# Performance work log

Hardware: AMD Instinct MI355X
Metric: run time of the kernel (lower is better)

## Reference

```python
import jax, jax.numpy as jnp
import numpy as np

FILTERS = 512
DQK = FILTERS // 8  # 64


def setup_inputs() -> dict:
    key = jax.random.key(0)
    ks = jax.random.split(key, 7)
    B, H, W, C = 32, 32, 32, FILTERS
    x = jax.random.normal(ks[0], (B, H, W, C), dtype=jnp.float32)
    # 1x1 convs == per-pixel dense layers: weight [Cin, Cout], bias [Cout]
    def glorot(k, cin, cout):
        lim = np.sqrt(6.0 / (cin + cout)).astype(np.float32)
        return jax.random.uniform(k, (cin, cout), jnp.float32, -lim, lim)
    return {
        "x": x,
        "wq": glorot(ks[1], C, DQK), "bq": jnp.zeros((DQK,), jnp.float32),
        "wk": glorot(ks[2], C, DQK), "bk": jnp.zeros((DQK,), jnp.float32),
        "wv": glorot(ks[3], C, C),   "bv": jnp.zeros((C,), jnp.float32),
    }


def reference(x, wq, bq, wk, bk, wv, bv):
    B, H, W, C = x.shape
    N = H * W
    xf = x.reshape(B, N, C)                       # flatten spatial -> tokens
    q = xf @ wq + bq                              # [B, N, C//8]
    k = xf @ wk + bk                              # [B, N, C//8]
    v = xf @ wv + bv                              # [B, N, C]
    scale = 1.0 / jnp.sqrt(jnp.float32(C // 8))
    scores = jnp.einsum('bnd,bmd->bnm', q, k) * scale  # [B, N, N]
    probs = jax.nn.softmax(scores, axis=-1)
    attended = jnp.einsum('bnm,bmc->bnc', probs, v)    # [B, N, C]
    return attended.reshape(B, H, W, C) + x
```

## Files before the change

### kernel.cpp

```cpp
#include <hip/hip_runtime.h>
#include <stdint.h>

#define B_ 32
#define N_ 1024
#define C_ 512
#define D_ 64

typedef __attribute__((ext_vector_type(8))) __bf16 bf8;
typedef __attribute__((ext_vector_type(4))) float f32x4;

typedef const __attribute__((address_space(1))) void* gp_t;
typedef __attribute__((address_space(3))) void* lp_t;

__device__ inline void g2l16(const void* g, void* l) {
    __builtin_amdgcn_global_load_lds((gp_t)g, (lp_t)l, 16, 0, 0);
}

__device__ inline float b2f(unsigned short u) {
    return __uint_as_float(((unsigned)u) << 16);
}
__device__ inline unsigned short f2b(float f) {
    unsigned u = __float_as_uint(f);
    u += 0x7FFF + ((u >> 16) & 1);
    return (unsigned short)(u >> 16);
}

#define MFMA16(a, b, c) __builtin_amdgcn_mfma_f32_16x16x32_bf16((a), (b), (c), 0, 0, 0)

__global__ __launch_bounds__(256) void xcvt(const float* __restrict__ x,
                                            unsigned short* __restrict__ xb) {
    int i = blockIdx.x * 256 + threadIdx.x;
    float4 f = ((const float4*)x)[i];
    ushort4 o;
    o.x = f2b(f.x); o.y = f2b(f.y); o.z = f2b(f.z); o.w = f2b(f.w);
    ((ushort4*)xb)[i] = o;
}

__global__ __launch_bounds__(256) void wtrans(const float* __restrict__ w,
                                              unsigned short* __restrict__ wt,
                                              int cout) {
    int t = blockIdx.x * 256 + threadIdx.x;
    int co = t >> 9;
    int ci = t & 511;
    wt[t] = f2b(w[(size_t)ci * cout + co]);
}

__global__ __launch_bounds__(256) void qkv(
    const unsigned short* __restrict__ xb,
    const unsigned short* __restrict__ WT,
    const float* __restrict__ bq, const float* __restrict__ bk,
    const float* __restrict__ bv,
    unsigned short* __restrict__ q, unsigned short* __restrict__ k,
    unsigned short* __restrict__ vT)
{
    const int rb = blockIdx.x;
    const int cb = blockIdx.y;
    const int tid = threadIdx.x;
    const int lane = tid & 63;
    const int wave = tid >> 6;
    const int wm = wave >> 1, wn = wave & 1;
    const int lr = lane & 15;
    const int lk = lane >> 4;

    __shared__ unsigned short SM[16896];
    unsigned short* As = SM;
    unsigned short* Bs = SM + 8192;
    unsigned short* TB = SM;

    const int row0 = rb * 128;
    const int col0 = cb * 128;

    f32x4 zero4 = {0.f, 0.f, 0.f, 0.f};
    f32x4 acc[4][4];
    #pragma unroll
    for (int i = 0; i < 4; ++i)
        #pragma unroll
        for (int j = 0; j < 4; ++j) acc[i][j] = zero4;

    for (int kk = 0; kk < C_; kk += 64) {
        __syncthreads();
        #pragma unroll
        for (int i = 0; i < 4; ++i) {
            int f = wave * 4 + i;
            int t = f >> 1, kq = f & 1;
            g2l16(xb + (size_t)(row0 + t * 16 + lr) * C_ + kk + kq * 32 + lk * 8,
                  &As[f * 512]);
            g2l16(WT + (size_t)(col0 + t * 16 + lr) * C_ + kk + kq * 32 + lk * 8,
                  &Bs[f * 512]);
        }
        __syncthreads();
        #pragma unroll
        for (int kq = 0; kq < 2; ++kq) {
            bf8 a[4], bb[4];
            #pragma unroll
            for (int ti = 0; ti < 4; ++ti)
                a[ti] = *(const bf8*)&As[((wm * 4 + ti) * 2 + kq) * 512 + lane * 8];
            #pragma unroll
            for (int tj = 0; tj < 4; ++tj)
                bb[tj] = *(const bf8*)&Bs[((wn * 4 + tj) * 2 + kq) * 512 + lane * 8];
            #pragma unroll
            for (int ti = 0; ti < 4; ++ti)
                #pragma unroll
                for (int tj = 0; tj < 4; ++tj)
                    acc[ti][tj] = MFMA16(a[ti], bb[tj], acc[ti][tj]);
        }
    }

    if (cb == 0) {
        unsigned short* outp = (wn == 0) ? q : k;
        const float* bias = (wn == 0) ? bq : bk;
        #pragma unroll
        for (int ti = 0; ti < 4; ++ti)
            #pragma unroll
            for (int tj = 0; tj < 4; ++tj) {
                int col = tj * 16 + lr;
                float bi = bias[col];
                #pragma unroll
                for (int r = 0; r < 4; ++r) {
                    int row = row0 + wm * 64 + ti * 16 + lk * 4 + r;
                    outp[(size_t)row * D_ + col] = f2b(acc[ti][tj][r] + bi);
                }
            }
    } else {
        const int colv = (cb - 1) * 128;
        __syncthreads();
        #pragma unroll
        for (int ti = 0; ti < 4; ++ti)
            #pragma unroll
            for (int tj = 0; tj < 4; ++tj) {
                int c = wn * 64 + tj * 16 + lr;
                float bi = bv[colv + c];
                int tok = wm * 64 + ti * 16 + lk * 4;
                ushort4 o;
                o.x = f2b(acc[ti][tj][0] + bi);
                o.y = f2b(acc[ti][tj][1] + bi);
                o.z = f2b(acc[ti][tj][2] + bi);
                o.w = f2b(acc[ti][tj][3] + bi);
                *(ushort4*)&TB[c * 132 + tok] = o;
            }
        __syncthreads();
        const int b  = row0 >> 10;
        const int n0 = row0 & 1023;
        #pragma unroll
        for (int i = 0; i < 16; ++i) {
            int idx = tid + 256 * i;
            int c = idx >> 5, ch = idx & 31;
            ushort4 t4 = *(const ushort4*)&TB[c * 132 + ch * 4];
            *(ushort4*)&vT[((size_t)(b * C_ + colv + c)) * N_ + n0 + ch * 4] = t4;
        }
    }
}

#define SLD 1032
__global__ __launch_bounds__(256) void scores(
    const unsigned short* __restrict__ q,
    const unsigned short* __restrict__ k,
    unsigned short* __restrict__ P)
{
    const int qt = blockIdx.x, b = blockIdx.y;
    const int tid = threadIdx.x, lane = tid & 63, wave = tid >> 6;
    const int lr = lane & 15, lk = lane >> 4;
    __shared__ unsigned short S[16 * SLD];

    const int n0 = qt * 16;
    const unsigned short* qrow = q + (size_t)(b * N_ + n0 + lr) * D_ + lk * 8;
    bf8 qa0 = *(const bf8*)(qrow);
    bf8 qa1 = *(const bf8*)(qrow + 32);

    const int m0w = wave * 256;
    #pragma unroll 4
    for (int mt = 0; mt < 16; ++mt) {
        int m = m0w + mt * 16;
        const unsigned short* krow = k + (size_t)(b * N_ + m + lr) * D_ + lk * 8;
        bf8 kb0 = *(const bf8*)(krow);
        bf8 kb1 = *(const bf8*)(krow + 32);
        f32x4 s = {0.f, 0.f, 0.f, 0.f};
        s = MFMA16(qa0, kb0, s);
        s = MFMA16(qa1, kb1, s);
        #pragma unroll
        for (int r = 0; r < 4; ++r)
            S[(lk * 4 + r) * SLD + m + lr] = f2b(s[r] * 0.125f);
    }
    __syncthreads();

    #pragma unroll
    for (int rr4 = 0; rr4 < 4; ++rr4) {
        int rr = wave * 4 + rr4;
        float vals[16];
        float mx = -1e30f;
        #pragma unroll
        for (int j = 0; j < 16; ++j) {
            vals[j] = b2f(S[rr * SLD + j * 64 + lane]);
            mx = fmaxf(mx, vals[j]);
        }
        #pragma unroll
        for (int off = 32; off; off >>= 1) mx = fmaxf(mx, __shfl_xor(mx, off));
        float sum = 0.f;
        #pragma unroll
        for (int j = 0; j < 16; ++j) { vals[j] = __expf(vals[j] - mx); sum += vals[j]; }
        #pragma unroll
        for (int off = 32; off; off >>= 1) sum += __shfl_xor(sum, off);
        float inv = 1.f / sum;
        unsigned short* pp = P + (size_t)(b * N_ + n0 + rr) * N_;
        #pragma unroll
        for (int j = 0; j < 16; ++j) pp[j * 64 + lane] = f2b(vals[j] * inv);
    }
}

__global__ __launch_bounds__(256) void pv(
    const unsigned short* __restrict__ P,
    const unsigned short* __restrict__ vT,
    const float* __restrict__ x,
    float* __restrict__ out)
{
    const int m0 = blockIdx.x * 128, c0 = blockIdx.y * 128, b = blockIdx.z;
    const int tid = threadIdx.x, lane = tid & 63, wave = tid >> 6;
    const int wm = wave >> 1, wn = wave & 1;
    const int lr = lane & 15, lk = lane >> 4;

    __shared__ unsigned short As[128 * 64];
    __shared__ unsigned short Bs[128 * 64];

    f32x4 zero4 = {0.f, 0.f, 0.f, 0.f};
    f32x4 acc[4][4];
    #pragma unroll
    for (int i = 0; i < 4; ++i)
        #pragma unroll
        for (int j = 0; j < 4; ++j) acc[i][j] = zero4;

    const unsigned short* Pb = P  + (size_t)b * N_ * N_;
    const unsigned short* Vb = vT + (size_t)b * C_ * N_;

    for (int kk = 0; kk < N_; kk += 64) {
        __syncthreads();
        #pragma unroll
        for (int i = 0; i < 4; ++i) {
            int f = wave * 4 + i;
            int t = f >> 1, kq = f & 1;
            g2l16(Pb + (size_t)(m0 + t * 16 + lr) * N_ + kk + kq * 32 + lk * 8,
                  &As[f * 512]);
            g2l16(Vb + (size_t)(c0 + t * 16 + lr) * N_ + kk + kq * 32 + lk * 8,
                  &Bs[f * 512]);
        }
        __syncthreads();
        #pragma unroll
        for (int kq = 0; kq < 2; ++kq) {
            bf8 a[4], bb[4];
            #pragma unroll
            for (int ti = 0; ti < 4; ++ti)
                a[ti] = *(const bf8*)&As[((wm * 4 + ti) * 2 + kq) * 512 + lane * 8];
            #pragma unroll
            for (int tj = 0; tj < 4; ++tj)
                bb[tj] = *(const bf8*)&Bs[((wn * 4 + tj) * 2 + kq) * 512 + lane * 8];
            #pragma unroll
            for (int ti = 0; ti < 4; ++ti)
                #pragma unroll
                for (int tj = 0; tj < 4; ++tj)
                    acc[ti][tj] = MFMA16(a[ti], bb[tj], acc[ti][tj]);
        }
    }

    #pragma unroll
    for (int ti = 0; ti < 4; ++ti)
        #pragma unroll
        for (int tj = 0; tj < 4; ++tj) {
            int col = c0 + wn * 64 + tj * 16 + lr;
            #pragma unroll
            for (int r = 0; r < 4; ++r) {
                int row = m0 + wm * 64 + ti * 16 + lk * 4 + r;
                size_t idx = (size_t)(b * N_ + row) * C_ + col;
                out[idx] = acc[ti][tj][r] + x[idx];
            }
        }
}

extern "C" void kernel_launch(void* const* d_in, const int* in_sizes, int n_in,
                              void* d_out, int out_size, void* d_ws, size_t ws_size,
                              hipStream_t stream) {
    (void)in_sizes; (void)n_in; (void)out_size; (void)ws_size;
    const float* xf = (const float*)d_in[0];
    const float* wq = (const float*)d_in[1];
    const float* bq = (const float*)d_in[2];
    const float* wk = (const float*)d_in[3];
    const float* bk = (const float*)d_in[4];
    const float* wv = (const float*)d_in[5];
    const float* bv = (const float*)d_in[6];
    float* out = (float*)d_out;

    char* ws = (char*)d_ws;
    unsigned short* qb  = (unsigned short*)(ws);
    unsigned short* kb  = (unsigned short*)(ws + 4194304);
    unsigned short* vTb = (unsigned short*)(ws + 8388608);
    unsigned short* WT  = (unsigned short*)(ws + 41943040);
    unsigned short* xb  = (unsigned short*)(ws + 42598400);
    unsigned short* Pb  = (unsigned short*)(ws + 41943040);

    xcvt<<<16384, 256, 0, stream>>>(xf, xb);
    wtrans<<<128, 256, 0, stream>>>(wq, WT, 64);
    wtrans<<<128, 256, 0, stream>>>(wk, WT + 64 * 512, 64);
    wtrans<<<1024, 256, 0, stream>>>(wv, WT + 128 * 512, 512);
    qkv<<<dim3(256, 5), 256, 0, stream>>>(xb, WT, bq, bk, bv, qb, kb, vTb);
    scores<<<dim3(64, 32), 256, 0, stream>>>(qb, kb, Pb);
    pv<<<dim3(8, 4, 32), 256, 0, stream>>>(Pb, vTb, xf, out);
}
```

Baseline: 294.7 us.

## Fuse scores, softmax and PV into one attention kernel keeping probabilities in LDS

The separate scores and pv kernels are merged into one attn kernel. Each block handles 32 query rows and keeps the unnormalized bf16 probabilities in shared memory, then multiplies them by V read straight from global memory. Row normalization is deferred to the epilogue, so the 64 MB P matrix is never written to or read back from HBM. Block indices are also remapped so that consecutive blocks in qkv and attn share a batch or row tile, which should improve L2 reuse. In exchange, the PV stage loads V without LDS staging and with less reuse per block, and the larger LDS footprint may lower occupancy.

Result: slower. 327.3 us (+11.0%).

```diff
diff --git a/kernel.cpp b/kernel.cpp
--- a/kernel.cpp
+++ b/kernel.cpp
@@ -8,6 +8,7 @@
 
 typedef __attribute__((ext_vector_type(8))) __bf16 bf8;
 typedef __attribute__((ext_vector_type(4))) float f32x4;
+typedef __attribute__((ext_vector_type(8))) unsigned short u16x8;
 
 typedef const __attribute__((address_space(1))) void* gp_t;
 typedef __attribute__((address_space(3))) void* lp_t;
@@ -53,8 +54,10 @@
     unsigned short* __restrict__ q, unsigned short* __restrict__ k,
     unsigned short* __restrict__ vT)
 {
-    const int rb = blockIdx.x;
-    const int cb = blockIdx.y;
+    const int L = blockIdx.x;
+    const int s = L >> 3;
+    const int rb = (L & 7) + 8 * (s / 5);
+    const int cb = s % 5;
     const int tid = threadIdx.x;
     const int lane = tid & 63;
     const int wave = tid >> 6;
@@ -152,126 +155,119 @@
 }
 
 #define SLD 1032
-__global__ __launch_bounds__(256) void scores(
+__global__ __launch_bounds__(256) void attn(
     const unsigned short* __restrict__ q,
     const unsigned short* __restrict__ k,
-    unsigned short* __restrict__ P)
-{
-    const int qt = blockIdx.x, b = blockIdx.y;
-    const int tid = threadIdx.x, lane = tid & 63, wave = tid >> 6;
-    const int lr = lane & 15, lk = lane >> 4;
-    __shared__ unsigned short S[16 * SLD];
-
-    const int n0 = qt * 16;
-    const unsigned short* qrow = q + (size_t)(b * N_ + n0 + lr) * D_ + lk * 8;
-    bf8 qa0 = *(const bf8*)(qrow);
-    bf8 qa1 = *(const bf8*)(qrow + 32);
-
-    const int m0w = wave * 256;
-    #pragma unroll 4
-    for (int mt = 0; mt < 16; ++mt) {
-        int m = m0w + mt * 16;
-        const unsigned short* krow = k + (size_t)(b * N_ + m + lr) * D_ + lk * 8;
-        bf8 kb0 = *(const bf8*)(krow);
-        bf8 kb1 = *(const bf8*)(krow + 32);
-        f32x4 s = {0.f, 0.f, 0.f, 0.f};
-        s = MFMA16(qa0, kb0, s);
-        s = MFMA16(qa1, kb1, s);
-        #pragma unroll
-        for (int r = 0; r < 4; ++r)
-            S[(lk * 4 + r) * SLD + m + lr] = f2b(s[r] * 0.125f);
-    }
-    __syncthreads();
-
-    #pragma unroll
-    for (int rr4 = 0; rr4 < 4; ++rr4) {
-        int rr = wave * 4 + rr4;
-        float vals[16];
-        float mx = -1e30f;
-        #pragma unroll
-        for (int j = 0; j < 16; ++j) {
-            vals[j] = b2f(S[rr * SLD + j * 64 + lane]);
-            mx = fmaxf(mx, vals[j]);
-        }
-        #pragma unroll
-        for (int off = 32; off; off >>= 1) mx = fmaxf(mx, __shfl_xor(mx, off));
-        float sum = 0.f;
-        #pragma unroll
-        for (int j = 0; j < 16; ++j) { vals[j] = __expf(vals[j] - mx); sum += vals[j]; }
-        #pragma unroll
-        for (int off = 32; off; off >>= 1) sum += __shfl_xor(sum, off);
-        float inv = 1.f / sum;
-        unsigned short* pp = P + (size_t)(b * N_ + n0 + rr) * N_;
-        #pragma unroll
-        for (int j = 0; j < 16; ++j) pp[j * 64 + lane] = f2b(vals[j] * inv);
-    }
-}
-
-__global__ __launch_bounds__(256) void pv(
-    const unsigned short* __restrict__ P,
     const unsigned short* __restrict__ vT,
     const float* __restrict__ x,
     float* __restrict__ out)
 {
-    const int m0 = blockIdx.x * 128, c0 = blockIdx.y * 128, b = blockIdx.z;
+    const int bid = blockIdx.x;
+    const int b   = (bid & 7) + 8 * (bid >> 8);
+    const int qt  = (bid >> 3) & 31;
+    const int n0  = qt * 32;
     const int tid = threadIdx.x, lane = tid & 63, wave = tid >> 6;
-    const int wm = wave >> 1, wn = wave & 1;
     const int lr = lane & 15, lk = lane >> 4;
 
-    __shared__ unsigned short As[128 * 64];
-    __shared__ unsigned short Bs[128 * 64];
-
+    __shared__ unsigned short S[32 * SLD];
+    __shared__ float inv_s[32];
+
+    bf8 qa[2][2];
+    #pragma unroll
+    for (int rt = 0; rt < 2; ++rt)
+        #pragma unroll
+        for (int kq = 0; kq < 2; ++kq)
+            qa[rt][kq] = *(const bf8*)&q[(size_t)(b * N_ + n0 + rt * 16 + lr) * D_
+                                         + kq * 32 + lk * 8];
+
+    const int m0w = wave * 256;
+    #pragma unroll 2
+    for (int mt2 = 0; mt2 < 8; ++mt2) {
+        #pragma unroll
+        for (int h = 0; h < 2; ++h) {
+            int m = m0w + mt2 * 32 + h * 16;
+            const unsigned short* kp = k + (size_t)(b * N_ + m + lr) * D_ + lk * 8;
+            bf8 kb0 = *(const bf8*)(kp);
+            bf8 kb1 = *(const bf8*)(kp + 32);
+            #pragma unroll
+            for (int rt = 0; rt < 2; ++rt) {
+                f32x4 s4 = {0.f, 0.f, 0.f, 0.f};
+                s4 = MFMA16(qa[rt][0], kb0, s4);
+                s4 = MFMA16(qa[rt][1], kb1, s4);
+                #pragma unroll
+                for (int r = 0; r < 4; ++r)
+                    S[(rt * 16 + lk * 4 + r) * SLD + m + lr] = f2b(s4[r] * 0.125f);
+            }
+        }
+    }
+    __syncthreads();
+
+    #pragma unroll
+    for (int i = 0; i < 8; ++i) {
+        int row = wave * 8 + i;
+        u16x8 a = *(const u16x8*)&S[row * SLD + lane * 16];
+        u16x8 c = *(const u16x8*)&S[row * SLD + lane * 16 + 8];
+        float v[16];
+        #pragma unroll
+        for (int j = 0; j < 8; ++j) { v[j] = b2f(a[j]); v[8 + j] = b2f(c[j]); }
+        float mx = v[0];
+        #pragma unroll
+        for (int j = 1; j < 16; ++j) mx = fmaxf(mx, v[j]);
+        #pragma unroll
+        for (int off = 32; off; off >>= 1) mx = fmaxf(mx, __shfl_xor(mx, off));
+        float sum = 0.f;
+        #pragma unroll
+        for (int j = 0; j < 16; ++j) { v[j] = __expf(v[j] - mx); sum += v[j]; }
+        #pragma unroll
+        for (int off = 32; off; off >>= 1) sum += __shfl_xor(sum, off);
+        u16x8 oa, oc;
+        #pragma unroll
+        for (int j = 0; j < 8; ++j) { oa[j] = f2b(v[j]); oc[j] = f2b(v[8 + j]); }
+        *(u16x8*)&S[row * SLD + lane * 16] = oa;
+        *(u16x8*)&S[row * SLD + lane * 16 + 8] = oc;
+        if (lane == 0) inv_s[row] = 1.f / sum;
+    }
+    __syncthreads();
+
+    const int cbase = wave * 128;
     f32x4 zero4 = {0.f, 0.f, 0.f, 0.f};
-    f32x4 acc[4][4];
-    #pragma unroll
-    for (int i = 0; i < 4; ++i)
-        #pragma unroll
-        for (int j = 0; j < 4; ++j) acc[i][j] = zero4;
-
-    const unsigned short* Pb = P  + (size_t)b * N_ * N_;
-    const unsigned short* Vb = vT + (size_t)b * C_ * N_;
-
-    for (int kk = 0; kk < N_; kk += 64) {
-        __syncthreads();
-        #pragma unroll
-        for (int i = 0; i < 4; ++i) {
-            int f = wave * 4 + i;
-            int t = f >> 1, kq = f & 1;
-            g2l16(Pb + (size_t)(m0 + t * 16 + lr) * N_ + kk + kq * 32 + lk * 8,
-                  &As[f * 512]);
-            g2l16(Vb + (size_t)(c0 + t * 16 + lr) * N_ + kk + kq * 32 + lk * 8,
-                  &Bs[f * 512]);
-        }
-        __syncthreads();
-        #pragma unroll
-        for (int kq = 0; kq < 2; ++kq) {
-            bf8 a[4], bb[4];
-            #pragma unroll
-            for (int ti = 0; ti < 4; ++ti)
-                a[ti] = *(const bf8*)&As[((wm * 4 + ti) * 2 + kq) * 512 + lane * 8];
-            #pragma unroll
-            for (int tj = 0; tj < 4; ++tj)
-                bb[tj] = *(const bf8*)&Bs[((wn * 4 + tj) * 2 + kq) * 512 + lane * 8];
-            #pragma unroll
-            for (int ti = 0; ti < 4; ++ti)
-                #pragma unroll
-                for (int tj = 0; tj < 4; ++tj)
-                    acc[ti][tj] = MFMA16(a[ti], bb[tj], acc[ti][tj]);
-        }
-    }
-
-    #pragma unroll
-    for (int ti = 0; ti < 4; ++ti)
-        #pragma unroll
-        for (int tj = 0; tj < 4; ++tj) {
-            int col = c0 + wn * 64 + tj * 16 + lr;
-            #pragma unroll
-            for (int r = 0; r < 4; ++r) {
-                int row = m0 + wm * 64 + ti * 16 + lk * 4 + r;
-                size_t idx = (size_t)(b * N_ + row) * C_ + col;
-                out[idx] = acc[ti][tj][r] + x[idx];
-            }
-        }
+    f32x4 acc[8][2];
+    #pragma unroll
+    for (int ct = 0; ct < 8; ++ct) { acc[ct][0] = zero4; acc[ct][1] = zero4; }
+
+    const unsigned short* Vb = vT + ((size_t)b * C_ + cbase) * N_;
+    #pragma unroll 2
+    for (int mt = 0; mt < 32; ++mt) {
+        const int m0 = mt * 32;
+        bf8 va[8];
+        #pragma unroll
+        for (int ct = 0; ct < 8; ++ct)
+            va[ct] = *(const bf8*)&Vb[(size_t)(ct * 16 + lr) * N_ + m0 + lk * 8];
+        bf8 pb0 = *(const bf8*)&S[lr * SLD + m0 + lk * 8];
+        bf8 pb1 = *(const bf8*)&S[(16 + lr) * SLD + m0 + lk * 8];
+        #pragma unroll
+        for (int ct = 0; ct < 8; ++ct) {
+            acc[ct][0] = MFMA16(va[ct], pb0, acc[ct][0]);
+            acc[ct][1] = MFMA16(va[ct], pb1, acc[ct][1]);
+        }
+    }
+
+    #pragma unroll
+    for (int rt = 0; rt < 2; ++rt) {
+        float invr = inv_s[rt * 16 + lr];
+        #pragma unroll
+        for (int ct = 0; ct < 8; ++ct) {
+            size_t base = (size_t)(b * N_ + n0 + rt * 16 + lr) * C_
+                        + cbase + ct * 16 + lk * 4;
+            float4 xr = *(const float4*)&x[base];
+            float4 o;
+            o.x = acc[ct][rt][0] * invr + xr.x;
+            o.y = acc[ct][rt][1] * invr + xr.y;
+            o.z = acc[ct][rt][2] * invr + xr.z;
+            o.w = acc[ct][rt][3] * invr + xr.w;
+            *(float4*)&out[base] = o;
+        }
+    }
 }
 
 extern "C" void kernel_launch(void* const* d_in, const int* in_sizes, int n_in,
@@ -293,13 +289,11 @@
     unsigned short* vTb = (unsigned short*)(ws + 8388608);
     unsigned short* WT  = (unsigned short*)(ws + 41943040);
     unsigned short* xb  = (unsigned short*)(ws + 42598400);
-    unsigned short* Pb  = (unsigned short*)(ws + 41943040);
 
     xcvt<<<16384, 256, 0, stream>>>(xf, xb);
     wtrans<<<128, 256, 0, stream>>>(wq, WT, 64);
     wtrans<<<128, 256, 0, stream>>>(wk, WT + 64 * 512, 64);
     wtrans<<<1024, 256, 0, stream>>>(wv, WT + 128 * 512, 512);
-    qkv<<<dim3(256, 5), 256, 0, stream>>>(xb, WT, bq, bk, bv, qb, kb, vTb);
-    scores<<<dim3(64, 32), 256, 0, stream>>>(qb, kb, Pb);
-    pv<<<dim3(8, 4, 32), 256, 0, stream>>>(Pb, vTb, xf, out);
-}
+    qkv<<<1280, 256, 0, stream>>>(xb, WT, bq, bk, bv, qb, kb, vTb);
+    attn<<<1024, 256, 0, stream>>>(qb, kb, vTb, xf, out);
+}
```
